# Performance work log

Hardware: AMD Instinct MI355X
Metric: run time of the kernel (lower is better)

The kernel has to match this reference:

```python
import jax, jax.numpy as jnp
import numpy as np

B, E, H, N = 16, 1024, 16, 2048
Eh = E // H   # head dim = 64
BH = B * H    # 256


def setup_inputs() -> dict:
    key = jax.random.key(0)
    ks = jax.random.split(key, 12)
    query = jax.random.normal(ks[0], (B, E), jnp.float32)
    key_in = jax.random.normal(ks[1], (B, E), jnp.float32)
    value = jax.random.normal(ks[2], (B, E), jnp.float32)
    # State as it would look in steady state: a_sum ~ O(N) positive,
    # q_mem stores already-scaled queries (small), k/v unit-ish scale.
    a_sum_mem = float(N) * (0.9 + 0.2 * jax.random.uniform(ks[3], (BH, N - 1), jnp.float32))
    av_mem = (0.1 * float(N)) * jax.random.normal(ks[4], (BH, N - 1, Eh), jnp.float32)
    q_mem = 0.06 * jax.random.normal(ks[5], (BH, N, Eh), jnp.float32)
    k_t_mem = 0.5 * jax.random.normal(ks[6], (BH, Eh, N), jnp.float32)
    v_mem = 0.5 * jax.random.normal(ks[7], (BH, N, Eh), jnp.float32)
    in_proj_weight = 0.02 * jax.random.normal(ks[8], (3 * E, E), jnp.float32)
    in_proj_bias = jnp.zeros((3 * E,), jnp.float32)
    out_proj_weight = 0.02 * jax.random.normal(ks[9], (E, E), jnp.float32)
    out_proj_bias = jnp.zeros((E,), jnp.float32)
    return dict(query=query, key=key_in, value=value,
                a_sum_mem=a_sum_mem, av_mem=av_mem, q_mem=q_mem,
                k_t_mem=k_t_mem, v_mem=v_mem,
                in_proj_weight=in_proj_weight, in_proj_bias=in_proj_bias,
                out_proj_weight=out_proj_weight, out_proj_bias=out_proj_bias)


def _sdpa_step(a_sum_mem, av_mem, q_mem, k_t_mem, v_mem, q_step, k_step, v_step):
    # Faithful port of _scaled_dot_product_attention_step.
    q_step = q_step / jnp.sqrt(jnp.float32(Eh))          # (BH, Eh)
    q_old = q_mem[:, 0]                                   # (BH, Eh)
    k_old = k_t_mem[:, :, 0]                              # (BH, Eh)
    q_sel = jnp.stack((q_old, q_step), axis=1)            # (BH, 2, Eh)
    k_sel = jnp.stack((k_old, k_step), axis=2)            # (BH, Eh, 2)
    a_tb = jnp.exp(jnp.einsum('bte,bes->bts', q_sel, k_t_mem[:, :, 1:]))  # (BH, 2, N-1)
    a_lr = jnp.exp(jnp.einsum('bne,bet->bnt', q_mem[:, 1:, :], k_sel))    # (BH, N-1, 2)
    a_br = jnp.exp(jnp.sum(q_step * k_step, axis=1))      # (BH,)
    a_sum = jnp.concatenate(
        [a_sum_mem + a_lr[:, :, 1] - a_lr[:, :, 0],
         (a_tb[:, 1].sum(axis=1) + a_br)[:, None]], axis=1)               # (BH, N)
    av_top = (av_mem
              - a_lr[:, :, 0, None] * v_mem[:, 0][:, None, :]
              + a_lr[:, :, 1, None] * v_step[:, None, :])                 # (BH, N-1, Eh)
    av_bot = jnp.einsum('bs,bse->be', a_tb[:, 1], v_mem[:, 1:]) + a_br[:, None] * v_step
    av = jnp.concatenate([av_top, av_bot[:, None, :]], axis=1)            # (BH, N, Eh)
    out = av / a_sum[..., None]
    new_state = (a_sum[:, 1:], av[:, 1:],
                 jnp.concatenate([q_mem[:, 1:], q_step[:, None, :]], axis=1),
                 jnp.concatenate([k_t_mem[:, :, 1:], k_step[:, :, None]], axis=2),
                 jnp.concatenate([v_mem[:, 1:], v_step[:, None, :]], axis=1))
    return out, new_state


def reference(query, key, value, a_sum_mem, av_mem, q_mem, k_t_mem, v_mem,
              in_proj_weight, in_proj_bias, out_proj_weight, out_proj_bias):
    # Packed in-projection (q/k/v chunks of the packed weight).
    w_q, w_k, w_v = jnp.split(in_proj_weight, 3, axis=0)
    b_q, b_k, b_v = jnp.split(in_proj_bias, 3)
    q = (query @ w_q.T + b_q).reshape(BH, Eh)   # head split: (B, H*Eh) -> (B*H, Eh)
    k = (key @ w_k.T + b_k).reshape(BH, Eh)
    v = (value @ w_v.T + b_v).reshape(BH, Eh)
    attn, new_state = _sdpa_step(a_sum_mem, av_mem, q_mem, k_t_mem, v_mem, q, k, v)
    # (BH, N, Eh) -> (N, BH, Eh) -> (N, B, E), then output projection.
    attn = attn.transpose(1, 0, 2).reshape(N, B, E)
    out = attn @ out_proj_weight.T + out_proj_bias    # (N, B, E)
    return (out,) + new_state
```

## Files before the change

kernel.cpp:

```cpp
#include <hip/hip_runtime.h>
#include <hip/hip_bf16.h>

constexpr int kB  = 16;
constexpr int kE  = 1024;
constexpr int kH  = 16;
constexpr int kN  = 2048;
constexpr int kEh = 64;
constexpr int kBH = 256;
constexpr int kM  = kN * kB;

typedef __bf16 bf16x8 __attribute__((ext_vector_type(8)));
typedef float  f32x4  __attribute__((ext_vector_type(4)));
typedef unsigned short u16x4 __attribute__((ext_vector_type(4)));

static __device__ __forceinline__ unsigned short bf16_bits(float f) {
  union { __hip_bfloat16 h; unsigned short u; } cv;
  cv.h = __float2bfloat16(f);
  return cv.u;
}

static __device__ __forceinline__ f32x4 nt_load4(const float* p) {
  return __builtin_nontemporal_load(reinterpret_cast<const f32x4*>(p));
}
static __device__ __forceinline__ void nt_store4(float* p, f32x4 v) {
  __builtin_nontemporal_store(v, reinterpret_cast<f32x4*>(p));
}

__global__ __launch_bounds__(256) void prep_kernel(
    const float* __restrict__ query, const float* __restrict__ key_in,
    const float* __restrict__ value, const float* __restrict__ W,
    const float* __restrict__ bias,
    float* __restrict__ q_step, float* __restrict__ k_step,
    float* __restrict__ v_step,
    const float* __restrict__ wo, __hip_bfloat16* __restrict__ wo_bf) {
  __shared__ float red[4][16];
  int bid = blockIdx.x;
  int tid = threadIdx.x;
  if (bid >= 3072) {
    int i4 = ((bid - 3072) * 256 + tid) * 4;
    f32x4 w4 = nt_load4(wo + i4);
    u16x4 o;
    o[0] = bf16_bits(w4[0]); o[1] = bf16_bits(w4[1]);
    o[2] = bf16_bits(w4[2]); o[3] = bf16_bits(w4[3]);
    *reinterpret_cast<u16x4*>(reinterpret_cast<unsigned short*>(wo_bf) + i4) = o;
    return;
  }
  int j   = bid;
  int mat = j >> 10;
  int col = j & 1023;
  const float* in = (mat == 0) ? query : ((mat == 1) ? key_in : value);
  const float* wrow = W + (size_t)j * kE;

  float4 w4 = reinterpret_cast<const float4*>(wrow)[tid];
  float part[16];
#pragma unroll
  for (int r = 0; r < 16; ++r) {
    float4 in4 = reinterpret_cast<const float4*>(in + (size_t)r * kE)[tid];
    part[r] = w4.x * in4.x + w4.y * in4.y + w4.z * in4.z + w4.w * in4.w;
  }
#pragma unroll
  for (int r = 0; r < 16; ++r) {
    float v = part[r];
    for (int off = 32; off > 0; off >>= 1) v += __shfl_down(v, off, 64);
    part[r] = v;
  }
  int wave = tid >> 6;
  int lane = tid & 63;
  if (lane == 0) {
#pragma unroll
    for (int r = 0; r < 16; ++r) red[wave][r] = part[r];
  }
  __syncthreads();
  if (tid < 16) {
    int r = tid;
    float v = red[0][r] + red[1][r] + red[2][r] + red[3][r] + bias[j];
    int h = col >> 6, eh = col & 63;
    int bh = r * kH + h;
    if (mat == 0)      q_step[bh * kEh + eh] = v * 0.125f;
    else if (mat == 1) k_step[bh * kEh + eh] = v;
    else               v_step[bh * kEh + eh] = v;
  }
}

__global__ __launch_bounds__(256) void stream_kernel(
    const float* __restrict__ q_mem, const float* __restrict__ av_mem,
    const float* __restrict__ a_sum_mem, const float* __restrict__ k_t_mem,
    const float* __restrict__ v_mem, const float* __restrict__ q_step,
    const float* __restrict__ k_step, const float* __restrict__ v_step,
    float* __restrict__ q_out, float* __restrict__ av_out,
    float* __restrict__ a_sum_out, float* __restrict__ k_t_out,
    float* __restrict__ v_out, float* __restrict__ top_sum,
    float* __restrict__ av_last, __hip_bfloat16* __restrict__ attn) {
  __shared__ float qs[64];
  __shared__ float tbuf[1024];
  __shared__ f32x4 redv[4][16];
  __shared__ float redt[4];

  int bid = blockIdx.x;
  int tid = threadIdx.x;
  int wave = tid >> 6, lane = tid & 63;

  if (bid < 8192) {
    int b = bid >> 5;
    int chunk = bid & 31;
    int g = lane >> 4, c = lane & 15;
    int b_ = b >> 4, h = b & 15;

    f32x4 kst  = *reinterpret_cast<const f32x4*>(k_step + (size_t)b * kEh + c * 4);
    f32x4 vst  = *reinterpret_cast<const f32x4*>(v_step + (size_t)b * kEh + c * 4);
    f32x4 vold = *reinterpret_cast<const f32x4*>(v_mem + (size_t)b * kN * kEh + c * 4);
    const float* kt0 = k_t_mem + (size_t)b * kEh * kN;
    f32x4 kold;
    kold[0] = kt0[(size_t)(4 * c + 0) * kN];
    kold[1] = kt0[(size_t)(4 * c + 1) * kN];
    kold[2] = kt0[(size_t)(4 * c + 2) * kN];
    kold[3] = kt0[(size_t)(4 * c + 3) * kN];

    unsigned short* attn_u = reinterpret_cast<unsigned short*>(attn);

    int jb = chunk * 64 + wave * 16;
#pragma unroll
    for (int it = 0; it < 4; ++it) {
      int j = jb + it * 4 + g;
      bool valid = (j <= kN - 2);
      int jc = valid ? j : (kN - 2);

      f32x4 q4 = nt_load4(q_mem + ((size_t)b * kN + (jc + 1)) * kEh + c * 4);
      float p0 = q4[0] * kold[0] + q4[1] * kold[1] + q4[2] * kold[2] + q4[3] * kold[3];
      float p1 = q4[0] * kst[0]  + q4[1] * kst[1]  + q4[2] * kst[2]  + q4[3] * kst[3];
#pragma unroll
      for (int off = 1; off < 16; off <<= 1) {
        p0 += __shfl_xor(p0, off, 64);
        p1 += __shfl_xor(p1, off, 64);
      }
      float a0 = __expf(p0);
      float a1 = __expf(p1);
      float asum = a_sum_mem[(size_t)b * (kN - 1) + jc] + a1 - a0;
      f32x4 av4 = nt_load4(av_mem + ((size_t)b * (kN - 1) + jc) * kEh + c * 4);
      f32x4 avv;
      avv[0] = av4[0] - a0 * vold[0] + a1 * vst[0];
      avv[1] = av4[1] - a0 * vold[1] + a1 * vst[1];
      avv[2] = av4[2] - a0 * vold[2] + a1 * vst[2];
      avv[3] = av4[3] - a0 * vold[3] + a1 * vst[3];

      if (valid) {
        nt_store4(q_out + ((size_t)b * kN + jc) * kEh + c * 4, q4);
        float inv = 1.0f / asum;
        u16x4 pk;
        pk[0] = bf16_bits(avv[0] * inv);
        pk[1] = bf16_bits(avv[1] * inv);
        pk[2] = bf16_bits(avv[2] * inv);
        pk[3] = bf16_bits(avv[3] * inv);
        *reinterpret_cast<u16x4*>(
            attn_u + ((size_t)jc * kB + b_) * kE + h * kEh + c * 4) = pk;
        if (j >= 1) {
          nt_store4(av_out + ((size_t)b * (kN - 1) + (jc - 1)) * kEh + c * 4, avv);
          if (c == 0) a_sum_out[(size_t)b * (kN - 1) + (jc - 1)] = asum;
        }
      }
    }
    return;
  }

  int id2 = bid - 8192;
  int b = id2 >> 1, chunk = id2 & 1;

  if (tid < 64) qs[tid] = q_step[b * kEh + tid];
  __syncthreads();

  int c4 = chunk * 1024 + tid * 4;
  bool last = (c4 + 4 >= kN);
  const float* src = k_t_mem + (size_t)b * kEh * kN;
  float* dst = k_t_out + (size_t)b * kEh * kN;

  f32x4 dot = {0.f, 0.f, 0.f, 0.f};
#pragma unroll 4
  for (int e = 0; e < 64; ++e) {
    f32x4 a = nt_load4(src + (size_t)e * kN + c4);
    float s3 = last ? 0.f
                    : __builtin_nontemporal_load(src + (size_t)e * kN + c4 + 4);
    f32x4 sh;
    sh[0] = a[1]; sh[1] = a[2]; sh[2] = a[3]; sh[3] = s3;
    nt_store4(dst + (size_t)e * kN + c4, sh);
    float q = qs[e];
    dot[0] += q * sh[0];
    dot[1] += q * sh[1];
    dot[2] += q * sh[2];
    dot[3] += q * sh[3];
  }
  float tx = __expf(dot[0]);
  float ty = __expf(dot[1]);
  float tz = __expf(dot[2]);
  float tw = last ? 0.f : __expf(dot[3]);

  tbuf[tid * 4 + 0] = tx;
  tbuf[tid * 4 + 1] = ty;
  tbuf[tid * 4 + 2] = tz;
  tbuf[tid * 4 + 3] = tw;

  float s = tx + ty + tz + tw;
  for (int off = 32; off > 0; off >>= 1) s += __shfl_xor(s, off, 64);
  if (lane == 0) redt[wave] = s;
  __syncthreads();
  if (tid == 0)
    atomicAdd(&top_sum[b], redt[0] + redt[1] + redt[2] + redt[3]);

  int g = lane >> 4, c = lane & 15;
  const float* vsrc = v_mem + (size_t)b * kN * kEh;
  float* vdst = v_out + (size_t)b * kN * kEh;

  f32x4 acc = {0.f, 0.f, 0.f, 0.f};
  int sbase = chunk * 1024 + wave * 256;
#pragma unroll 4
  for (int it = 0; it < 64; ++it) {
    int s4 = sbase + it * 4 + g;
    bool valid = (s4 <= kN - 2);
    int sc = valid ? s4 : (kN - 2);
    float t = valid ? tbuf[s4 - chunk * 1024] : 0.f;
    f32x4 vv = nt_load4(vsrc + (size_t)(sc + 1) * kEh + c * 4);
    acc[0] += t * vv[0];
    acc[1] += t * vv[1];
    acc[2] += t * vv[2];
    acc[3] += t * vv[3];
    if (valid) nt_store4(vdst + (size_t)sc * kEh + c * 4, vv);
  }
#pragma unroll
  for (int off = 16; off <= 32; off <<= 1) {
    acc[0] += __shfl_xor(acc[0], off, 64);
    acc[1] += __shfl_xor(acc[1], off, 64);
    acc[2] += __shfl_xor(acc[2], off, 64);
    acc[3] += __shfl_xor(acc[3], off, 64);
  }
  if (g == 0) redv[wave][c] = acc;
  __syncthreads();
  if (tid < 16) {
    f32x4 a0 = redv[0][tid];
    f32x4 a1 = redv[1][tid];
    f32x4 a2 = redv[2][tid];
    f32x4 a3 = redv[3][tid];
    float* dstl = av_last + (size_t)b * kEh + tid * 4;
    atomicAdd(dstl + 0, a0[0] + a1[0] + a2[0] + a3[0]);
    atomicAdd(dstl + 1, a0[1] + a1[1] + a2[1] + a3[1]);
    atomicAdd(dstl + 2, a0[2] + a1[2] + a2[2] + a3[2]);
    atomicAdd(dstl + 3, a0[3] + a1[3] + a2[3] + a3[3]);
  }
}

__global__ __launch_bounds__(64) void final_kernel(
    const float* __restrict__ q_step, const float* __restrict__ k_step,
    const float* __restrict__ v_step, const float* __restrict__ top_sum,
    const float* __restrict__ av_last_in, float* __restrict__ q_out,
    float* __restrict__ k_t_out, float* __restrict__ v_out,
    float* __restrict__ a_sum_out, float* __restrict__ av_out,
    __hip_bfloat16* __restrict__ attn) {
  int b = blockIdx.x;
  int lane = threadIdx.x;
  int b_ = b >> 4, h = b & 15;
  float qs = q_step[b * kEh + lane];
  float ks = k_step[b * kEh + lane];
  float vs = v_step[b * kEh + lane];
  float p = qs * ks;
  for (int off = 32; off > 0; off >>= 1) p += __shfl_xor(p, off, 64);
  float abr = __expf(p);
  float asum = top_sum[b] + abr;
  float avl = av_last_in[b * kEh + lane] + abr * vs;
  attn[((size_t)(kN - 1) * kB + b_) * kE + h * kEh + lane] =
      __float2bfloat16(avl / asum);
  if (lane == 0) a_sum_out[(size_t)b * (kN - 1) + (kN - 2)] = asum;
  av_out[((size_t)b * (kN - 1) + (kN - 2)) * kEh + lane] = avl;
  q_out[((size_t)b * kN + (kN - 1)) * kEh + lane] = qs;
  k_t_out[(size_t)b * kEh * kN + (size_t)lane * kN + (kN - 1)] = ks;
  v_out[((size_t)b * kN + (kN - 1)) * kEh + lane] = vs;
}

#define GBM 256
#define GBN 256
#define GBK 64
#define GKT (kE / GBK)

__global__ __launch_bounds__(512, 2) void gemm_kernel(
    const __bf16* __restrict__ A, const __bf16* __restrict__ Bw,
    const float* __restrict__ bias, float* __restrict__ C) {
  __shared__ __bf16 lds[2][2][GBM * GBK];

  int tid = threadIdx.x;
  int wid = tid >> 6;
  int lane = tid & 63;

  int bid = blockIdx.x;
  int swz = (bid & 7) * 64 + (bid >> 3);
  int mt = swz >> 2;
  int nt = swz & 3;
  int m0 = mt * GBM;
  int n0 = nt * GBN;

  int wm = (wid >> 2) * 128;
  int wn = (wid & 3) * 64;

  int quad = lane >> 4;
  int mrow = lane & 15;

  f32x4 acc[8][4];
#pragma unroll
  for (int i = 0; i < 8; ++i)
#pragma unroll
    for (int j = 0; j < 4; ++j) acc[i][j] = (f32x4){0.f, 0.f, 0.f, 0.f};

  int srow = tid >> 3;
  int scol = (tid & 7) * 8;
  const __bf16* gA = A + (size_t)(m0 + srow) * kE + scol;
  const __bf16* gB = Bw + (size_t)(n0 + srow) * kE + scol;

  auto stage = [&](int t) {
    int buf = t & 1;
    int k0 = t * GBK;
#pragma unroll
    for (int q = 0; q < 4; ++q) {
      __builtin_amdgcn_global_load_lds(
          (const __attribute__((address_space(1))) void*)(gA + (size_t)q * 64 * kE + k0),
          (__attribute__((address_space(3))) void*)((char*)&lds[buf][0][0] + q * 8192 + tid * 16),
          16, 0, 0);
      __builtin_amdgcn_global_load_lds(
          (const __attribute__((address_space(1))) void*)(gB + (size_t)q * 64 * kE + k0),
          (__attribute__((address_space(3))) void*)((char*)&lds[buf][1][0] + q * 8192 + tid * 16),
          16, 0, 0);
    }
  };

  stage(0);

  for (int t = 0; t < GKT; ++t) {
    if (t + 1 < GKT) stage(t + 1);
    if (t + 1 < GKT) {
      asm volatile("s_waitcnt vmcnt(8)" ::: "memory");
    } else {
      asm volatile("s_waitcnt vmcnt(0)" ::: "memory");
    }
    __builtin_amdgcn_s_barrier();

    const __bf16* la = &lds[t & 1][0][0];
    const __bf16* lb = &lds[t & 1][1][0];
#pragma unroll
    for (int kk = 0; kk < 2; ++kk) {
      bf16x8 bfr[4];
#pragma unroll
      for (int j = 0; j < 4; ++j)
        bfr[j] = *(const bf16x8*)(lb + (wn + j * 16 + mrow) * GBK + kk * 32 + quad * 8);
#pragma unroll
      for (int i = 0; i < 8; ++i) {
        bf16x8 af = *(const bf16x8*)(la + (wm + i * 16 + mrow) * GBK + kk * 32 + quad * 8);
#pragma unroll
        for (int j = 0; j < 4; ++j)
          acc[i][j] = __builtin_amdgcn_mfma_f32_16x16x32_bf16(af, bfr[j], acc[i][j], 0, 0, 0);
      }
    }
    __builtin_amdgcn_s_barrier();
  }

  int colq = lane & 15;
  int rowq = (lane >> 4) * 4;
#pragma unroll
  for (int i = 0; i < 8; ++i) {
#pragma unroll
    for (int j = 0; j < 4; ++j) {
      int col = n0 + wn + j * 16 + colq;
      float bv = bias[col];
      size_t base = (size_t)(m0 + wm + i * 16 + rowq) * kE + col;
#pragma unroll
      for (int r = 0; r < 4; ++r) {
        __builtin_nontemporal_store(acc[i][j][r] + bv, &C[base + (size_t)r * kE]);
      }
    }
  }
}

extern "C" void kernel_launch(void* const* d_in, const int* in_sizes, int n_in,
                              void* d_out, int out_size, void* d_ws,
                              size_t ws_size, hipStream_t stream) {
  const float* query          = (const float*)d_in[0];
  const float* key_in         = (const float*)d_in[1];
  const float* value          = (const float*)d_in[2];
  const float* a_sum_mem      = (const float*)d_in[3];
  const float* av_mem         = (const float*)d_in[4];
  const float* q_mem          = (const float*)d_in[5];
  const float* k_t_mem        = (const float*)d_in[6];
  const float* v_mem          = (const float*)d_in[7];
  const float* in_proj_weight = (const float*)d_in[8];
  const float* in_proj_bias   = (const float*)d_in[9];
  const float* out_proj_weight= (const float*)d_in[10];
  const float* out_proj_bias  = (const float*)d_in[11];

  float* out       = (float*)d_out;
  float* a_sum_out = out + (size_t)kN * kB * kE;
  float* av_out    = a_sum_out + (size_t)kBH * (kN - 1);
  float* q_out     = av_out + (size_t)kBH * (kN - 1) * kEh;
  float* k_t_out   = q_out + (size_t)kBH * kN * kEh;
  float* v_out     = k_t_out + (size_t)kBH * kEh * kN;

  char* ws = (char*)d_ws;
  float* q_step  = (float*)ws;
  float* k_step  = q_step + 16384;
  float* v_step  = k_step + 16384;
  float* top_sum = v_step + 16384;
  float* av_last = top_sum + 256;
  __hip_bfloat16* wo_bf   = (__hip_bfloat16*)(ws + 2359296);
  __hip_bfloat16* attn_bf = (__hip_bfloat16*)(ws + 4456448);

  hipMemsetAsync(ws + 196608, 0, 66560, stream);

  prep_kernel<<<4096, 256, 0, stream>>>(query, key_in, value, in_proj_weight,
                                        in_proj_bias, q_step, k_step, v_step,
                                        out_proj_weight, wo_bf);
  stream_kernel<<<8704, 256, 0, stream>>>(q_mem, av_mem, a_sum_mem, k_t_mem,
                                          v_mem, q_step, k_step, v_step, q_out,
                                          av_out, a_sum_out, k_t_out, v_out,
                                          top_sum, av_last, attn_bf);
  final_kernel<<<kBH, 64, 0, stream>>>(q_step, k_step, v_step, top_sum,
                                       av_last, q_out, k_t_out, v_out,
                                       a_sum_out, av_out, attn_bf);
  gemm_kernel<<<(kM / GBM) * (kE / GBN), 512, 0, stream>>>(
      (const __bf16*)attn_bf, (const __bf16*)wo_bf, out_proj_bias, out);
}
```

Before: 1.114 ms.

## Stage GEMM epilogue through LDS for vectorized stores; fold memset into prep kernel

The GEMM epilogue now writes accumulator fragments into shared memory and reads them back as contiguous rows, so each thread issues 16-byte nontemporal stores of full row segments instead of scattered scalar stores. Separately, the workspace memset is removed and its zeroing is done by 65 extra blocks in the prep kernel, saving one launch. The epilogue adds eight rounds of barrier plus LDS round-trips, and it reuses the operand LDS buffer, whose size must be large enough for the padded staging tile.

Result: no change. 1.108 ms (-0.6%).

```diff
diff --git a/kernel.cpp b/kernel.cpp
--- a/kernel.cpp
+++ b/kernel.cpp
@@ -32,10 +32,15 @@
     const float* __restrict__ bias,
     float* __restrict__ q_step, float* __restrict__ k_step,
     float* __restrict__ v_step,
-    const float* __restrict__ wo, __hip_bfloat16* __restrict__ wo_bf) {
+    const float* __restrict__ wo, __hip_bfloat16* __restrict__ wo_bf,
+    float* __restrict__ zero_base) {
   __shared__ float red[4][16];
   int bid = blockIdx.x;
   int tid = threadIdx.x;
+  if (bid >= 4096) {
+    zero_base[(bid - 4096) * 256 + tid] = 0.f;
+    return;
+  }
   if (bid >= 3072) {
     int i4 = ((bid - 3072) * 256 + tid) * 4;
     f32x4 w4 = nt_load4(wo + i4);
@@ -357,19 +362,34 @@
     __builtin_amdgcn_s_barrier();
   }
 
+  float* cst = reinterpret_cast<float*>(&lds[0][0][0]);
   int colq = lane & 15;
-  int rowq = (lane >> 4) * 4;
+  int rowq = lane >> 4;
+  float bv[4];
+#pragma unroll
+  for (int j = 0; j < 4; ++j) bv[j] = bias[n0 + wn + j * 16 + colq];
+
+  int lrow_base = (wm >> 7) * 16 + rowq * 4;
+  int r_t = tid >> 4;
+  int c4 = (tid & 15) * 4;
+  int grow = m0 + (r_t >> 4) * 128 + (r_t & 15);
+
 #pragma unroll
   for (int i = 0; i < 8; ++i) {
+    __syncthreads();
 #pragma unroll
     for (int j = 0; j < 4; ++j) {
-      int col = n0 + wn + j * 16 + colq;
-      float bv = bias[col];
-      size_t base = (size_t)(m0 + wm + i * 16 + rowq) * kE + col;
-#pragma unroll
-      for (int r = 0; r < 4; ++r) {
-        __builtin_nontemporal_store(acc[i][j][r] + bv, &C[base + (size_t)r * kE]);
-      }
+      int cw = wn + j * 16 + colq;
+#pragma unroll
+      for (int r = 0; r < 4; ++r)
+        cst[(lrow_base + r) * 260 + cw] = acc[i][j][r] + bv[j];
+    }
+    __syncthreads();
+    size_t gbase = (size_t)(grow + i * 16) * kE + n0 + c4;
+#pragma unroll
+    for (int k4 = 0; k4 < 4; ++k4) {
+      f32x4 vv = *reinterpret_cast<const f32x4*>(&cst[r_t * 260 + c4 + k4 * 64]);
+      __builtin_nontemporal_store(vv, reinterpret_cast<f32x4*>(&C[gbase + (size_t)k4 * 64]));
     }
   }
 }
@@ -406,11 +426,9 @@
   __hip_bfloat16* wo_bf   = (__hip_bfloat16*)(ws + 2359296);
   __hip_bfloat16* attn_bf = (__hip_bfloat16*)(ws + 4456448);
 
-  hipMemsetAsync(ws + 196608, 0, 66560, stream);
-
-  prep_kernel<<<4096, 256, 0, stream>>>(query, key_in, value, in_proj_weight,
+  prep_kernel<<<4161, 256, 0, stream>>>(query, key_in, value, in_proj_weight,
                                         in_proj_bias, q_step, k_step, v_step,
-                                        out_proj_weight, wo_bf);
+                                        out_proj_weight, wo_bf, top_sum);
   stream_kernel<<<8704, 256, 0, stream>>>(q_mem, av_mem, a_sum_mem, k_t_mem,
                                           v_mem, q_step, k_step, v_step, q_out,
                                           av_out, a_sum_out, k_t_out, v_out,
```
